# Kernel tuning notes

Measured on AMD Instinct MI355X. Metric: run time of the kernel, lower is better.

The kernel has to match this reference:

```python
import math
import jax, jax.numpy as jnp
import numpy as np

B, S, D = 4, 2048, 512
H = 8
HD = D // H  # 64


def setup_inputs() -> dict:
    key = jax.random.key(0)
    k1, k2, k3, k4, k5 = jax.random.split(key, 5)
    x = jax.random.normal(k1, (B, S, D), dtype=jnp.float32)
    # additive causal mask, broadcast over [H, B, S, S] in the original code
    neg_inf = jnp.float32(-1e9)
    mask = jnp.where(jnp.tril(jnp.ones((S, S), dtype=bool)), 0.0, neg_inf).astype(jnp.float32)
    Wqkv = jax.random.normal(k2, (D, 3 * D), dtype=jnp.float32) * (1.0 / math.sqrt(D))
    bqkv = jax.random.normal(k3, (3 * D,), dtype=jnp.float32) * 0.02
    Wo = jax.random.normal(k4, (D, D), dtype=jnp.float32) * (1.0 / math.sqrt(D))
    bo = jax.random.normal(k5, (D,), dtype=jnp.float32) * 0.02
    return {"x": x, "mask": mask, "Wqkv": Wqkv, "bqkv": bqkv, "Wo": Wo, "bo": bo}


def reference(x, mask, Wqkv, bqkv, Wo, bo):
    b, s, d = x.shape
    hd = d // H
    qkv = x @ Wqkv + bqkv                       # [b, s, 3d]
    # match torch: reshape to [b, s, H, 3*hd], move heads, chunk last dim
    qkv = qkv.reshape(b, s, H, 3 * hd).transpose(0, 2, 1, 3)  # [b, H, s, 3hd]
    q, k, v = jnp.split(qkv, 3, axis=-1)        # each [b, H, s, hd]
    scale = 1.0 / math.sqrt(hd)
    scores = jnp.einsum('bhqd,bhkd->bhqk', q, k) * scale
    scores = scores + mask                      # mask [s, s] broadcasts over [b, H, s, s]
    attn = jax.nn.softmax(scores, axis=-1)
    vals = jnp.einsum('bhqk,bhkd->bhqd', attn, v)
    vals = vals.transpose(0, 2, 1, 3).reshape(b, s, d)
    return vals @ Wo + bo
```

## Files before the change

kernel.cpp:

```cpp
#include <hip/hip_runtime.h>
#include <hip/hip_bf16.h>

#define S_ 2048
#define D_ 512
#define HD_ 64
#define HH_ 8
#define M_ 8192

typedef __attribute__((ext_vector_type(8))) short short8;
typedef __attribute__((ext_vector_type(4))) short short4v;
typedef __attribute__((ext_vector_type(4))) float f32x4;

__device__ __forceinline__ unsigned short f2bf(float f) {
  unsigned u = __builtin_bit_cast(unsigned, f);
  u += 0x7fffu + ((u >> 16) & 1u);
  return (unsigned short)(u >> 16);
}

__device__ __forceinline__ f32x4 mfma16(short8 a, short8 b, f32x4 c) {
  return __builtin_amdgcn_mfma_f32_16x16x32_bf16(a, b, c, 0, 0, 0);
}

#define GLOAD_LDS16(gp, lp)                                                        \
  __builtin_amdgcn_global_load_lds(                                                \
      (const __attribute__((address_space(1))) void*)(gp),                         \
      (__attribute__((address_space(3))) void*)(lp), 16, 0, 0)


__global__ __launch_bounds__(256) void k_cvt_bf16x8(const float* __restrict__ x,
                                                    short* __restrict__ o) {
  int idx = blockIdx.x * 256 + threadIdx.x;
  const float4* p = (const float4*)x;
  float4 a = p[idx * 2];
  float4 b = p[idx * 2 + 1];
  short8 v;
  v[0] = (short)f2bf(a.x); v[1] = (short)f2bf(a.y);
  v[2] = (short)f2bf(a.z); v[3] = (short)f2bf(a.w);
  v[4] = (short)f2bf(b.x); v[5] = (short)f2bf(b.y);
  v[6] = (short)f2bf(b.z); v[7] = (short)f2bf(b.w);
  *(short8*)&o[idx * 8] = v;
}

__global__ __launch_bounds__(256) void k_cvt_transpose(const float* __restrict__ w,
                                                       short* __restrict__ wt,
                                                       int C) {
  __shared__ short T[32][33];
  const int tx = threadIdx.x & 31, ty = threadIdx.x >> 5;
  const int n0 = blockIdx.x * 32, k0 = blockIdx.y * 32;
#pragma unroll
  for (int i = 0; i < 4; i++) {
    int k = k0 + ty + 8 * i;
    T[ty + 8 * i][tx] = (short)f2bf(w[k * C + n0 + tx]);
  }
  __syncthreads();
#pragma unroll
  for (int i = 0; i < 4; i++) {
    int n = n0 + ty + 8 * i;
    wt[n * 512 + k0 + tx] = T[tx][ty + 8 * i];
  }
}

template <int MODE>
__global__ __launch_bounds__(256) void k_gemm(const short* __restrict__ A,
                                              const short* __restrict__ Bt,
                                              const float* __restrict__ bias,
                                              short* __restrict__ Qo,
                                              short* __restrict__ Ko,
                                              short* __restrict__ VTo,
                                              float* __restrict__ Fo) {
  __shared__ short As[4096];
  __shared__ short Bs[4096];
  const int tid = threadIdx.x;
  const int w = tid >> 6, l = tid & 63, g = l >> 4, c = l & 15;
  const int bm = blockIdx.x * 128, bn = blockIdx.y * 128;
  const int wm = (w >> 1) * 64, wn = (w & 1) * 64;
  const int ch = w * 64 + l;
  const int ar = ch >> 2;
  const int ac = (ch & 3) * 8;
  f32x4 acc[4][4] = {};
  const short* Ap = A + (bm + ar) * 512 + ac;
  const short* Ap2 = Ap + 64 * 512;
  const short* Bp = Bt + (bn + ar) * 512 + ac;
  const short* Bp2 = Bp + 64 * 512;
  short* AsW = &As[w * 512];
  short* BsW = &Bs[w * 512];

  for (int k0 = 0; k0 < 512; k0 += 32) {
    __syncthreads();
    GLOAD_LDS16(Ap + k0, AsW);
    GLOAD_LDS16(Ap2 + k0, AsW + 2048);
    GLOAD_LDS16(Bp + k0, BsW);
    GLOAD_LDS16(Bp2 + k0, BsW + 2048);
    __syncthreads();
    short8 af[4], bfr[4];
#pragma unroll
    for (int mt = 0; mt < 4; mt++)
      af[mt] = *(const short8*)&As[(wm + mt * 16 + c) * 32 + 8 * g];
#pragma unroll
    for (int nt = 0; nt < 4; nt++)
      bfr[nt] = *(const short8*)&Bs[(wn + nt * 16 + c) * 32 + 8 * g];
#pragma unroll
    for (int mt = 0; mt < 4; mt++)
#pragma unroll
      for (int nt = 0; nt < 4; nt++)
        acc[mt][nt] = mfma16(af[mt], bfr[nt], acc[mt][nt]);
  }

  if (MODE == 0) {
    const float QS = 0.125f * 1.4426950408889634f;
#pragma unroll
    for (int nt = 0; nt < 4; nt++) {
      int n = bn + wn + nt * 16 + c;
      float bv = bias[n];
      int h = n / 192;
      int t = n - h * 192;
      int type = t >> 6;
      int hd = t & 63;
      float sc = (type == 0) ? QS : 1.0f;
#pragma unroll
      for (int mt = 0; mt < 4; mt++) {
        int m0 = bm + wm + mt * 16 + 4 * g;
        int b = m0 >> 11, s0 = m0 & 2047;
        int bh = b * 8 + h;
        if (type == 2) {
          int sw = (s0 & ~63) | (((((s0 >> 3) & 7) ^ (hd & 7)) << 3)) | (s0 & 7);
          short4v pk;
#pragma unroll
          for (int r = 0; r < 4; r++) pk[r] = (short)f2bf(acc[mt][nt][r] + bv);
          *(short4v*)&VTo[(bh * 64 + hd) * 2048 + sw] = pk;
        } else if (type == 1) {
#pragma unroll
          for (int r = 0; r < 4; r++) {
            int s = s0 + r;
            int hds = ((((hd >> 3) ^ (s & 7)) << 3)) | (hd & 7);
            Ko[(bh * 2048 + s) * 64 + hds] = (short)f2bf(acc[mt][nt][r] + bv);
          }
        } else {
#pragma unroll
          for (int r = 0; r < 4; r++)
            Qo[(bh * 2048 + s0 + r) * 64 + hd] = (short)f2bf((acc[mt][nt][r] + bv) * sc);
        }
      }
    }
  } else {
#pragma unroll
    for (int nt = 0; nt < 4; nt++) {
      int n = bn + wn + nt * 16 + c;
      float bv = bias[n];
#pragma unroll
      for (int mt = 0; mt < 4; mt++) {
        int m0 = bm + wm + mt * 16 + 4 * g;
#pragma unroll
        for (int r = 0; r < 4; r++) Fo[(m0 + r) * 512 + n] = acc[mt][nt][r] + bv;
      }
    }
  }
}

__global__ __launch_bounds__(256, 4) void k_attn(const short* __restrict__ Q,
                                                 const short* __restrict__ K,
                                                 const short* __restrict__ VT,
                                                 short* __restrict__ ctx) {
  __shared__ short Ks[2][4096];
  __shared__ short Vs[2][4096];
  __shared__ short P[4][1024];
  const int tid = threadIdx.x;
  const int w = tid >> 6, l = tid & 63, g = l >> 4, c = l & 15;

  const int x = blockIdx.x;
  const int bh = x & 31;
  const int jc = 31 - (x >> 5);
  const int qbase = jc * 64 + w * 16;
  const int ntiles = jc + 1;

  const short* Qb = Q + bh * S_ * HD_;
  const short* Kb = K + bh * S_ * HD_;
  const short* Vb = VT + bh * HD_ * S_;

  const int i0 = tid, i1 = tid + 256;
  const int kr0 = i0 >> 3, kc0 = (i0 & 7) * 8;
  const int kr1 = i1 >> 3, kc1 = (i1 & 7) * 8;
  short* KL0 = &Ks[0][w * 512];
  short* KL1 = &Ks[0][2048 + w * 512];
  short* VL0 = &Vs[0][w * 512];
  short* VL1 = &Vs[0][2048 + w * 512];

#define STAGE(buf, kv0)                                                     \
  {                                                                         \
    GLOAD_LDS16(Kb + ((kv0) + kr0) * 64 + kc0, KL0 + (buf)*4096);           \
    GLOAD_LDS16(Kb + ((kv0) + kr1) * 64 + kc1, KL1 + (buf)*4096);           \
    GLOAD_LDS16(Vb + kr0 * 2048 + (kv0) + kc0, VL0 + (buf)*4096);           \
    GLOAD_LDS16(Vb + kr1 * 2048 + (kv0) + kc1, VL1 + (buf)*4096);           \
  }

  short* Pw = &P[w][0];
  const int bb = bh >> 3, hh = bh & 7;
  const f32x4 CINIT = {-16.f, -16.f, -16.f, -16.f};

  short8 qf0 = *(const short8*)&Qb[(qbase + c) * 64 + 8 * g];
  short8 qf1 = *(const short8*)&Qb[(qbase + c) * 64 + 8 * g + 32];

  f32x4 o[4];
  float psum[4];
#pragma unroll
  for (int nt = 0; nt < 4; nt++) o[nt] = f32x4{0.f, 0.f, 0.f, 0.f};
#pragma unroll
  for (int r = 0; r < 4; r++) psum[r] = 0.f;

  STAGE(0, 0);
  __syncthreads();

  int cur = 0;
  for (int it = 0; it < ntiles; ++it) {
    const int kv0 = it * 64;
    if (it + 1 < ntiles) STAGE(cur ^ 1, kv0 + 64);

    const short* Kt = &Ks[cur][0];
    const short* Vt = &Vs[cur][0];

    f32x4 sa[4];
#pragma unroll
    for (int nt = 0; nt < 4; nt++) {
      short8 kf0 = *(const short8*)&Kt[((nt * 16 + c) << 6) + ((g ^ (c & 7)) << 3)];
      short8 kf1 = *(const short8*)&Kt[((nt * 16 + c) << 6) + (((g + 4) ^ (c & 7)) << 3)];
      sa[nt] = mfma16(qf0, kf0, CINIT);
      sa[nt] = mfma16(qf1, kf1, sa[nt]);
    }

    if (kv0 + 64 > qbase) {
#pragma unroll
      for (int nt = 0; nt < 4; nt++) {
        int kv = kv0 + nt * 16 + c;
#pragma unroll
        for (int r = 0; r < 4; r++) {
          int qrow = qbase + 4 * g + r;
          if (kv > qrow) sa[nt][r] = -1e30f;
        }
      }
    }

#pragma unroll
    for (int nt = 0; nt < 4; nt++)
#pragma unroll
      for (int r = 0; r < 4; r++) {
        float pv = __builtin_amdgcn_exp2f(sa[nt][r]);
        psum[r] += pv;
        int row = 4 * g + r;
        int col = nt * 16 + c;
        int off = (row << 6) + ((((col >> 3) ^ (row & 7)) << 3)) + (col & 7);
        Pw[off] = (short)f2bf(pv);
      }

#pragma unroll
    for (int kvb = 0; kvb < 2; kvb++) {
      short8 pa = *(const short8*)&Pw[(c << 6) + (((kvb * 4 + g) ^ (c & 7)) << 3)];
#pragma unroll
      for (int nt = 0; nt < 4; nt++) {
        short8 vb = *(const short8*)&Vt[((nt * 16 + c) << 6) +
                                        (((kvb * 4 + g) ^ (c & 7)) << 3)];
        o[nt] = mfma16(pa, vb, o[nt]);
      }
    }

    __syncthreads();
    cur ^= 1;
  }

#pragma unroll
  for (int off = 1; off < 16; off <<= 1)
#pragma unroll
    for (int r = 0; r < 4; r++) psum[r] += __shfl_xor(psum[r], off, 64);

  float inv[4];
#pragma unroll
  for (int r = 0; r < 4; r++) inv[r] = 1.0f / psum[r];
#pragma unroll
  for (int nt = 0; nt < 4; nt++)
#pragma unroll
    for (int r = 0; r < 4; r++) {
      int srow = qbase + 4 * g + r;
      ctx[(bb * S_ + srow) * 512 + hh * 64 + nt * 16 + c] =
          (short)f2bf(o[nt][r] * inv[r]);
    }
#undef STAGE
}


extern "C" void kernel_launch(void* const* d_in, const int* in_sizes, int n_in,
                              void* d_out, int out_size, void* d_ws, size_t ws_size,
                              hipStream_t stream) {
  const float* x = (const float*)d_in[0];
  const float* Wqkv = (const float*)d_in[2];
  const float* bqkv = (const float*)d_in[3];
  const float* Wo = (const float*)d_in[4];
  const float* bo = (const float*)d_in[5];
  float* out = (float*)d_out;

  char* ws = (char*)d_ws;
  short* xb    = (short*)(ws + 0);
  short* wqkvt = (short*)(ws + 8388608);
  short* wot   = (short*)(ws + 9961472);
  short* Qw    = (short*)(ws + 10485760);
  short* Kw    = (short*)(ws + 18874368);
  short* VTw   = (short*)(ws + 27262976);
  short* ctx   = (short*)(ws + 35651584);

  k_cvt_bf16x8<<<2048, 256, 0, stream>>>(x, xb);
  {
    dim3 gt(48, 16);
    k_cvt_transpose<<<gt, 256, 0, stream>>>(Wqkv, wqkvt, 1536);
    dim3 gt2(16, 16);
    k_cvt_transpose<<<gt2, 256, 0, stream>>>(Wo, wot, 512);
  }

  dim3 g1(64, 12);
  k_gemm<0><<<g1, 256, 0, stream>>>(xb, wqkvt, bqkv, Qw, Kw, VTw, nullptr);

  k_attn<<<1024, 256, 0, stream>>>(Qw, Kw, VTw, ctx);

  dim3 g3(64, 4);
  k_gemm<1><<<g3, 256, 0, stream>>>(ctx, wot, bo, nullptr, nullptr, nullptr, out);
}
```

Measured before the change: 94.09 us.

## Double-buffer GEMM K-tiles with pre-swizzled global layouts for conflict-free LDS reads

The GEMM now uses K=64 tiles with two LDS buffers, so the next tile's global-to-LDS loads are issued before the current tile's MFMAs run, and the per-iteration barriers drop from two to one. To keep LDS fragment reads free of bank conflicts without an extra pass, the producers (the x conversion, the weight transpose and the attention ctx store) write their bf16 outputs with an XOR swizzle in 8-element groups inside each 64-wide chunk, and the GEMM reads with the matching swizzle. LDS use grows fourfold to 64KB per block, which may limit occupancy.

After: 88.79 us. 5.6% less time.

```diff
diff --git a/kernel.cpp b/kernel.cpp
--- a/kernel.cpp
+++ b/kernel.cpp
@@ -25,7 +25,6 @@
   __builtin_amdgcn_global_load_lds(                                                \
       (const __attribute__((address_space(1))) void*)(gp),                         \
       (__attribute__((address_space(3))) void*)(lp), 16, 0, 0)
-
 
 __global__ __launch_bounds__(256) void k_cvt_bf16x8(const float* __restrict__ x,
                                                     short* __restrict__ o) {
@@ -38,7 +37,9 @@
   v[2] = (short)f2bf(a.z); v[3] = (short)f2bf(a.w);
   v[4] = (short)f2bf(b.x); v[5] = (short)f2bf(b.y);
   v[6] = (short)f2bf(b.z); v[7] = (short)f2bf(b.w);
-  *(short8*)&o[idx * 8] = v;
+  int row = idx >> 6;
+  int dst = row * 512 + ((idx >> 3) & 7) * 64 + (((idx & 7) ^ (row & 7)) << 3);
+  *(short8*)&o[dst] = v;
 }
 
 __global__ __launch_bounds__(256) void k_cvt_transpose(const float* __restrict__ w,
@@ -56,7 +57,9 @@
 #pragma unroll
   for (int i = 0; i < 4; i++) {
     int n = n0 + ty + 8 * i;
-    wt[n * 512 + k0 + tx] = T[tx][ty + 8 * i];
+    int k = k0 + tx;
+    int ksw = (k & ~63) | ((((k >> 3) & 7) ^ (n & 7)) << 3) | (k & 7);
+    wt[n * 512 + ksw] = T[tx][ty + 8 * i];
   }
 }
 
@@ -68,43 +71,63 @@
                                               short* __restrict__ Ko,
                                               short* __restrict__ VTo,
                                               float* __restrict__ Fo) {
-  __shared__ short As[4096];
-  __shared__ short Bs[4096];
+  __shared__ short As[2][8192];
+  __shared__ short Bs[2][8192];
   const int tid = threadIdx.x;
   const int w = tid >> 6, l = tid & 63, g = l >> 4, c = l & 15;
   const int bm = blockIdx.x * 128, bn = blockIdx.y * 128;
   const int wm = (w >> 1) * 64, wn = (w & 1) * 64;
-  const int ch = w * 64 + l;
-  const int ar = ch >> 2;
-  const int ac = (ch & 3) * 8;
   f32x4 acc[4][4] = {};
-  const short* Ap = A + (bm + ar) * 512 + ac;
-  const short* Ap2 = Ap + 64 * 512;
-  const short* Bp = Bt + (bn + ar) * 512 + ac;
-  const short* Bp2 = Bp + 64 * 512;
-  short* AsW = &As[w * 512];
-  short* BsW = &Bs[w * 512];
-
-  for (int k0 = 0; k0 < 512; k0 += 32) {
+  const int sr = l >> 3, sc8 = (l & 7) * 8;
+  const short* Ap = A + (bm + sr) * 512 + sc8;
+  const short* Bp = Bt + (bn + sr) * 512 + sc8;
+  const int s0 = w * 4;
+
+#define GSTAGE(buf, k0)                                                      \
+  {                                                                          \
+    GLOAD_LDS16(Ap + (s0 + 0) * 4096 + (k0), &As[buf][(s0 + 0) * 512]);      \
+    GLOAD_LDS16(Ap + (s0 + 1) * 4096 + (k0), &As[buf][(s0 + 1) * 512]);     \
+    GLOAD_LDS16(Ap + (s0 + 2) * 4096 + (k0), &As[buf][(s0 + 2) * 512]);     \
+    GLOAD_LDS16(Ap + (s0 + 3) * 4096 + (k0), &As[buf][(s0 + 3) * 512]);     \
+    GLOAD_LDS16(Bp + (s0 + 0) * 4096 + (k0), &Bs[buf][(s0 + 0) * 512]);     \
+    GLOAD_LDS16(Bp + (s0 + 1) * 4096 + (k0), &Bs[buf][(s0 + 1) * 512]);     \
+    GLOAD_LDS16(Bp + (s0 + 2) * 4096 + (k0), &Bs[buf][(s0 + 2) * 512]);     \
+    GLOAD_LDS16(Bp + (s0 + 3) * 4096 + (k0), &Bs[buf][(s0 + 3) * 512]);     \
+  }
+
+  GSTAGE(0, 0);
+  __syncthreads();
+
+  const int cs = c & 7;
+  int cur = 0;
+  for (int k0 = 0; k0 < 512; k0 += 64) {
+    if (k0 + 64 < 512) GSTAGE(cur ^ 1, k0 + 64);
+
+    short8 a0[4], a1[4], b0[4], b1[4];
+#pragma unroll
+    for (int mt = 0; mt < 4; mt++) {
+      const short* r = &As[cur][(wm + mt * 16 + c) * 64];
+      a0[mt] = *(const short8*)&r[(g ^ cs) << 3];
+      a1[mt] = *(const short8*)&r[((g + 4) ^ cs) << 3];
+    }
+#pragma unroll
+    for (int nt = 0; nt < 4; nt++) {
+      const short* r = &Bs[cur][(wn + nt * 16 + c) * 64];
+      b0[nt] = *(const short8*)&r[(g ^ cs) << 3];
+      b1[nt] = *(const short8*)&r[((g + 4) ^ cs) << 3];
+    }
+#pragma unroll
+    for (int mt = 0; mt < 4; mt++)
+#pragma unroll
+      for (int nt = 0; nt < 4; nt++) {
+        acc[mt][nt] = mfma16(a0[mt], b0[nt], acc[mt][nt]);
+        acc[mt][nt] = mfma16(a1[mt], b1[nt], acc[mt][nt]);
+      }
+
     __syncthreads();
-    GLOAD_LDS16(Ap + k0, AsW);
-    GLOAD_LDS16(Ap2 + k0, AsW + 2048);
-    GLOAD_LDS16(Bp + k0, BsW);
-    GLOAD_LDS16(Bp2 + k0, BsW + 2048);
-    __syncthreads();
-    short8 af[4], bfr[4];
-#pragma unroll
-    for (int mt = 0; mt < 4; mt++)
-      af[mt] = *(const short8*)&As[(wm + mt * 16 + c) * 32 + 8 * g];
-#pragma unroll
-    for (int nt = 0; nt < 4; nt++)
-      bfr[nt] = *(const short8*)&Bs[(wn + nt * 16 + c) * 32 + 8 * g];
-#pragma unroll
-    for (int mt = 0; mt < 4; mt++)
-#pragma unroll
-      for (int nt = 0; nt < 4; nt++)
-        acc[mt][nt] = mfma16(af[mt], bfr[nt], acc[mt][nt]);
-  }
+    cur ^= 1;
+  }
+#undef GSTAGE
 
   if (MODE == 0) {
     const float QS = 0.125f * 1.4426950408889634f;
@@ -120,10 +143,10 @@
 #pragma unroll
       for (int mt = 0; mt < 4; mt++) {
         int m0 = bm + wm + mt * 16 + 4 * g;
-        int b = m0 >> 11, s0 = m0 & 2047;
+        int b = m0 >> 11, ss = m0 & 2047;
         int bh = b * 8 + h;
         if (type == 2) {
-          int sw = (s0 & ~63) | (((((s0 >> 3) & 7) ^ (hd & 7)) << 3)) | (s0 & 7);
+          int sw = (ss & ~63) | (((((ss >> 3) & 7) ^ (hd & 7)) << 3)) | (ss & 7);
           short4v pk;
 #pragma unroll
           for (int r = 0; r < 4; r++) pk[r] = (short)f2bf(acc[mt][nt][r] + bv);
@@ -131,14 +154,14 @@
         } else if (type == 1) {
 #pragma unroll
           for (int r = 0; r < 4; r++) {
-            int s = s0 + r;
+            int s = ss + r;
             int hds = ((((hd >> 3) ^ (s & 7)) << 3)) | (hd & 7);
             Ko[(bh * 2048 + s) * 64 + hds] = (short)f2bf(acc[mt][nt][r] + bv);
           }
         } else {
 #pragma unroll
           for (int r = 0; r < 4; r++)
-            Qo[(bh * 2048 + s0 + r) * 64 + hd] = (short)f2bf((acc[mt][nt][r] + bv) * sc);
+            Qo[(bh * 2048 + ss + r) * 64 + hd] = (short)f2bf((acc[mt][nt][r] + bv) * sc);
         }
       }
     }
@@ -279,8 +302,8 @@
 #pragma unroll
     for (int r = 0; r < 4; r++) {
       int srow = qbase + 4 * g + r;
-      ctx[(bb * S_ + srow) * 512 + hh * 64 + nt * 16 + c] =
-          (short)f2bf(o[nt][r] * inv[r]);
+      int colsw = hh * 64 + (((nt * 2 + (c >> 3)) ^ (srow & 7)) << 3) + (c & 7);
+      ctx[(bb * S_ + srow) * 512 + colsw] = (short)f2bf(o[nt][r] * inv[r]);
     }
 #undef STAGE
 }
```
